# Kernel optimization log

Hardware: AMD Instinct MI355X
Metric: run time of the kernel (lower is better)

Reference implementation:

```python
import jax, jax.numpy as jnp
import numpy as np
import math

JOINT_NAMES = ['pelvis', 'hip_R', 'hip_L', 'knee_R', 'knee_L', 'ankle_R', 'ankle_L', 'trunk', 'shoulder_R', 'shoulder_L', 'elbow_R', 'elbow_L']
KINEMATIC_CHAINS = {'pelvis': ['hip_R', 'hip_L', 'trunk'], 'hip_R': ['pelvis', 'knee_R'], 'hip_L': ['pelvis', 'knee_L'], 'knee_R': ['hip_R', 'ankle_R'], 'knee_L': ['hip_L', 'ankle_L'], 'ankle_R': ['knee_R'], 'ankle_L': ['knee_L'], 'trunk': ['pelvis', 'shoulder_R', 'shoulder_L'], 'shoulder_R': ['trunk', 'elbow_R'], 'shoulder_L': ['trunk', 'elbow_L'], 'elbow_R': ['shoulder_R'], 'elbow_L': ['shoulder_L']}

D_MODEL = 128
N_HEADS = 4
HEAD_DIM = D_MODEL // N_HEADS
B = 16384
N = 12

def build_adjacency_matrix():
    n = len(JOINT_NAMES)
    adj = np.zeros((n, n), dtype=np.float32)
    idx = {name: i for i, name in enumerate(JOINT_NAMES)}
    for joint, neighbors in KINEMATIC_CHAINS.items():
        i = idx[joint]
        for nb in neighbors:
            j = idx[nb]
            adj[i, j] = 1.0
            adj[j, i] = 1.0
    adj = adj + np.eye(n, dtype=np.float32)
    return jnp.asarray(adj)

def setup_inputs() -> dict:
    key = jax.random.key(0)
    ks = jax.random.split(key, 12)
    s = 1.0 / math.sqrt(D_MODEL)  # torch Linear default init scale
    inp = {
        'x': jax.random.normal(ks[0], (B, N, D_MODEL), dtype=jnp.float32),
        'visibility': jax.random.uniform(ks[1], (B, N), dtype=jnp.float32),
        'Wq': jax.random.uniform(ks[2], (D_MODEL, D_MODEL), jnp.float32, -s, s),
        'bq': jax.random.uniform(ks[3], (D_MODEL,), jnp.float32, -s, s),
        'Wk': jax.random.uniform(ks[4], (D_MODEL, D_MODEL), jnp.float32, -s, s),
        'bk': jax.random.uniform(ks[5], (D_MODEL,), jnp.float32, -s, s),
        'Wv': jax.random.uniform(ks[6], (D_MODEL, D_MODEL), jnp.float32, -s, s),
        'bv': jax.random.uniform(ks[7], (D_MODEL,), jnp.float32, -s, s),
        'Wo': jax.random.uniform(ks[8], (D_MODEL, D_MODEL), jnp.float32, -s, s),
        'bo': jax.random.uniform(ks[9], (D_MODEL,), jnp.float32, -s, s),
        'bias_scale': jnp.asarray(1.0, dtype=jnp.float32),
        'adjacency': build_adjacency_matrix(),
    }
    return inp

def reference(x, visibility, Wq, bq, Wk, bk, Wv, bv, Wo, bo, bias_scale, adjacency):
    Bsz, Nj, D = x.shape
    # projections; weights stored as (out,in) like torch Linear -> x @ W.T + b
    def proj(W, b):
        return (jnp.einsum('bnd,ed->bne', x, W) + b).reshape(Bsz, Nj, N_HEADS, HEAD_DIM).transpose(0, 2, 1, 3)
    q = proj(Wq, bq)  # (B, H, N, hd)
    k = proj(Wk, bk)
    v = proj(Wv, bv)
    scores = jnp.einsum('bhnd,bhmd->bhnm', q, k) / math.sqrt(HEAD_DIM)
    scores = scores + adjacency[None, None, :, :] * bias_scale
    # visibility mask: subtract 10 where key joint is not visible
    scores = scores - 10.0 * (1.0 - visibility[:, None, None, :])
    attn = jax.nn.softmax(scores, axis=-1)
    out = jnp.einsum('bhnm,bhmd->bhnd', attn, v)
    out = out.transpose(0, 2, 1, 3).reshape(Bsz, Nj, D)
    out = jnp.einsum('bnd,ed->bne', out, Wo) + bo
    return out
```

## Files before the change

kernel.cpp:

```cpp
#include <hip/hip_runtime.h>


typedef unsigned short u16;
typedef short bf16x8 __attribute__((ext_vector_type(8)));
typedef float f32x4 __attribute__((ext_vector_type(4)));

#define MFMA(a, b, c) __builtin_amdgcn_mfma_f32_16x16x32_bf16((a), (b), (c), 0, 0, 0)

#define BPW   4
#define ROWS  (BPW * 12)
#define XPAD  136

struct SMem {
    u16   xs[ROWS * XPAD];
    u16   qs[ROWS * XPAD];
    u16   ks[ROWS * XPAD];
    u16   vT[BPW * 128 * 32];
    u16   P[4 * 16 * 32];
    float bias_s[16 * 16];
    float vis_s[BPW * 16];
    float bvec[4 * 128];
};

__device__ __forceinline__ u16 f2b(float f) {
    unsigned u = __builtin_bit_cast(unsigned, f);
    return (u16)((u + 0x7fffu + ((u >> 16) & 1u)) >> 16);
}

__device__ __forceinline__ void st4(u16* p, float a, float b, float c, float d) {
    ushort4 v; v.x = f2b(a); v.y = f2b(b); v.z = f2b(c); v.w = f2b(d);
    *(ushort4*)p = v;
}

__global__ void prep_w(const float* __restrict__ Wq, const float* __restrict__ Wk,
                       const float* __restrict__ Wv, const float* __restrict__ Wo,
                       u16* __restrict__ wbf) {
    int i = blockIdx.x * 256 + threadIdx.x;
    wbf[i]         = f2b(Wq[i]);
    wbf[16384 + i] = f2b(Wk[i]);
    wbf[32768 + i] = f2b(Wv[i]);
    wbf[49152 + i] = f2b(Wo[i]);
}

__global__ __launch_bounds__(256, 2) void cja_main(
    const float* __restrict__ x, const float* __restrict__ vis,
    const float* __restrict__ bq, const float* __restrict__ bk,
    const float* __restrict__ bv, const float* __restrict__ bo,
    const float* __restrict__ bias_scale, const float* __restrict__ adj,
    const u16* __restrict__ wbf, float* __restrict__ out)
{
    extern __shared__ char smraw[];
    SMem& sm = *(SMem*)smraw;

    const int tid  = threadIdx.x;
    const int wave = tid >> 6;
    const int lane = tid & 63;
    const int lq   = lane >> 4;
    const int lm   = lane & 15;
    const int b0   = blockIdx.x * BPW;

    for (int i = tid; i < ROWS * 32; i += 256) {
        int row = i >> 5, c4 = (i & 31) << 2;
        float4 v = *(const float4*)(x + ((size_t)(b0 * 12 + row) << 7) + c4);
        st4(sm.xs + row * XPAD + c4, v.x, v.y, v.z, v.w);
    }
    for (int i = tid; i < BPW * 128; i += 256) {
        unsigned* d = (unsigned*)(sm.vT + i * 32 + 12);
        #pragma unroll
        for (int j = 0; j < 10; j++) d[j] = 0u;
    }
    if (tid < 64) {
        unsigned* d = (unsigned*)(sm.P + tid * 32 + 16);
        #pragma unroll
        for (int j = 0; j < 8; j++) d[j] = 0u;
    }
    {
        float scale = bias_scale[0];
        int n = tid >> 4, m = tid & 15;
        float bval = -1e30f;
        if (n < 12 && m < 12) bval = adj[n * 12 + m] * scale;
        sm.bias_s[tid] = bval;
        if (tid < BPW * 16) {
            int bb = tid >> 4, mm = tid & 15;
            sm.vis_s[tid] = (mm < 12) ? vis[(size_t)(b0 + bb) * 12 + mm] : 1.0f;
        }
        if (tid < 128) {
            sm.bvec[tid]       = bq[tid];
            sm.bvec[128 + tid] = bk[tid];
            sm.bvec[256 + tid] = bv[tid];
            sm.bvec[384 + tid] = bo[tid];
        }
    }
    __syncthreads();

    {
        const u16* Wq_b = wbf;
        const u16* Wk_b = wbf + 16384;
        const u16* Wv_b = wbf + 32768;
        f32x4 accq[2][3], acck[2][3], accv[3][2];
        #pragma unroll
        for (int i = 0; i < 2; i++)
            #pragma unroll
            for (int j = 0; j < 3; j++) { accq[i][j] = (f32x4){0,0,0,0}; acck[i][j] = (f32x4){0,0,0,0}; }
        #pragma unroll
        for (int i = 0; i < 3; i++)
            #pragma unroll
            for (int j = 0; j < 2; j++) accv[i][j] = (f32x4){0,0,0,0};

        const int mrow0 = (wave * 2) * 16 + lm;
        const int mrow1 = mrow0 + 16;
        #pragma unroll
        for (int ks = 0; ks < 4; ks++) {
            const int koff = ks * 32 + lq * 8;
            bf16x8 xf[3];
            #pragma unroll
            for (int nt = 0; nt < 3; nt++)
                xf[nt] = *(const bf16x8*)(sm.xs + (nt * 16 + lm) * XPAD + koff);
            bf16x8 wq0 = *(const bf16x8*)(Wq_b + mrow0 * 128 + koff);
            bf16x8 wq1 = *(const bf16x8*)(Wq_b + mrow1 * 128 + koff);
            bf16x8 wk0 = *(const bf16x8*)(Wk_b + mrow0 * 128 + koff);
            bf16x8 wk1 = *(const bf16x8*)(Wk_b + mrow1 * 128 + koff);
            bf16x8 wv0 = *(const bf16x8*)(Wv_b + mrow0 * 128 + koff);
            bf16x8 wv1 = *(const bf16x8*)(Wv_b + mrow1 * 128 + koff);
            #pragma unroll
            for (int nt = 0; nt < 3; nt++) {
                accq[0][nt] = MFMA(wq0, xf[nt], accq[0][nt]);
                accq[1][nt] = MFMA(wq1, xf[nt], accq[1][nt]);
                acck[0][nt] = MFMA(wk0, xf[nt], acck[0][nt]);
                acck[1][nt] = MFMA(wk1, xf[nt], acck[1][nt]);
                accv[nt][0] = MFMA(xf[nt], wv0, accv[nt][0]);
                accv[nt][1] = MFMA(xf[nt], wv1, accv[nt][1]);
            }
        }
        #pragma unroll
        for (int mi = 0; mi < 2; mi++) {
            const int e0 = (wave * 2 + mi) * 16 + lq * 4;
            float bq0 = sm.bvec[e0], bq1 = sm.bvec[e0+1], bq2 = sm.bvec[e0+2], bq3 = sm.bvec[e0+3];
            float bk0 = sm.bvec[128+e0], bk1 = sm.bvec[128+e0+1], bk2 = sm.bvec[128+e0+2], bk3 = sm.bvec[128+e0+3];
            #pragma unroll
            for (int nt = 0; nt < 3; nt++) {
                const int n = nt * 16 + lm;
                st4(sm.qs + n * XPAD + e0, accq[mi][nt][0]+bq0, accq[mi][nt][1]+bq1,
                                           accq[mi][nt][2]+bq2, accq[mi][nt][3]+bq3);
                st4(sm.ks + n * XPAD + e0, acck[mi][nt][0]+bk0, acck[mi][nt][1]+bk1,
                                           acck[mi][nt][2]+bk2, acck[mi][nt][3]+bk3);
            }
        }
        #pragma unroll
        for (int nt2 = 0; nt2 < 2; nt2++) {
            const int e = (wave * 2 + nt2) * 16 + lm;
            const float bvv = sm.bvec[256 + e];
            #pragma unroll
            for (int mt = 0; mt < 3; mt++) {
                #pragma unroll
                for (int r = 0; r < 4; r++) {
                    int n = mt * 16 + lq * 4 + r;
                    int bb = n / 12, j = n - bb * 12;
                    sm.vT[bb * 4096 + e * 32 + j] = f2b(accv[mt][nt2][r] + bvv);
                }
            }
        }
    }
    __syncthreads();

    {
        const int bl = wave;
        const int nql  = (lm < 12) ? lm : 11;
        const int qrow = (bl * 12 + nql) * XPAD;
        const float vism = 10.0f * (1.0f - sm.vis_s[bl * 16 + lm]);
        u16* Pw = sm.P + wave * 512;
        #pragma unroll
        for (int h = 0; h < 4; h++) {
            bf16x8 qa = *(const bf16x8*)(sm.qs + qrow + h * 32 + lq * 8);
            bf16x8 kb = *(const bf16x8*)(sm.ks + qrow + h * 32 + lq * 8);
            f32x4 sc = (f32x4){0,0,0,0};
            sc = MFMA(qa, kb, sc);
            float p[4];
            #pragma unroll
            for (int r = 0; r < 4; r++) {
                const int n = lq * 4 + r;
                float s = sc[r] * 0.17677669529663689f + sm.bias_s[n * 16 + lm] - vism;
                float mx = s;
                mx = fmaxf(mx, __shfl_xor(mx, 1, 16));
                mx = fmaxf(mx, __shfl_xor(mx, 2, 16));
                mx = fmaxf(mx, __shfl_xor(mx, 4, 16));
                mx = fmaxf(mx, __shfl_xor(mx, 8, 16));
                float e = __expf(s - mx);
                float l = e;
                l += __shfl_xor(l, 1, 16);
                l += __shfl_xor(l, 2, 16);
                l += __shfl_xor(l, 4, 16);
                l += __shfl_xor(l, 8, 16);
                p[r] = e / l;
            }
            #pragma unroll
            for (int r = 0; r < 4; r++)
                Pw[(lq * 4 + r) * 32 + lm] = (lm < 12) ? f2b(p[r]) : (u16)0;
            #pragma unroll
            for (int mt = 0; mt < 2; mt++) {
                bf16x8 va = *(const bf16x8*)(sm.vT + bl * 4096 + (h * 32 + mt * 16 + lm) * 32 + lq * 8);
                bf16x8 pb = *(const bf16x8*)(Pw + lm * 32 + lq * 8);
                f32x4 c = (f32x4){0,0,0,0};
                c = MFMA(va, pb, c);
                if (lm < 12) {
                    u16* d = sm.xs + (bl * 12 + lm) * XPAD + h * 32 + mt * 16 + lq * 4;
                    st4(d, c[0], c[1], c[2], c[3]);
                }
            }
        }
    }
    __syncthreads();

    {
        const u16* Wo_b = wbf + 49152;
        f32x4 acc[2][3];
        #pragma unroll
        for (int i = 0; i < 2; i++)
            #pragma unroll
            for (int j = 0; j < 3; j++) acc[i][j] = (f32x4){0,0,0,0};
        const int m0 = (wave * 2) * 16 + lm;
        #pragma unroll
        for (int ks = 0; ks < 4; ks++) {
            const int koff = ks * 32 + lq * 8;
            bf16x8 a0 = *(const bf16x8*)(Wo_b + m0 * 128 + koff);
            bf16x8 a1 = *(const bf16x8*)(Wo_b + (m0 + 16) * 128 + koff);
            #pragma unroll
            for (int nt = 0; nt < 3; nt++) {
                bf16x8 bfr = *(const bf16x8*)(sm.xs + (nt * 16 + lm) * XPAD + koff);
                acc[0][nt] = MFMA(a0, bfr, acc[0][nt]);
                acc[1][nt] = MFMA(a1, bfr, acc[1][nt]);
            }
        }
        #pragma unroll
        for (int mi = 0; mi < 2; mi++) {
            const int e0 = (wave * 2 + mi) * 16 + lq * 4;
            float bo0 = sm.bvec[384+e0], bo1 = sm.bvec[384+e0+1],
                  bo2 = sm.bvec[384+e0+2], bo3 = sm.bvec[384+e0+3];
            #pragma unroll
            for (int nt = 0; nt < 3; nt++) {
                const int n = nt * 16 + lm;
                float4 o;
                o.x = acc[mi][nt][0] + bo0;
                o.y = acc[mi][nt][1] + bo1;
                o.z = acc[mi][nt][2] + bo2;
                o.w = acc[mi][nt][3] + bo3;
                *(float4*)(out + ((size_t)(b0 * 12 + n) << 7) + e0) = o;
            }
        }
    }
}

extern "C" void kernel_launch(void* const* d_in, const int* in_sizes, int n_in,
                              void* d_out, int out_size, void* d_ws, size_t ws_size,
                              hipStream_t stream) {
    const float* x   = (const float*)d_in[0];
    const float* vis = (const float*)d_in[1];
    const float* Wq  = (const float*)d_in[2];
    const float* bq  = (const float*)d_in[3];
    const float* Wk  = (const float*)d_in[4];
    const float* bk  = (const float*)d_in[5];
    const float* Wv  = (const float*)d_in[6];
    const float* bv  = (const float*)d_in[7];
    const float* Wo  = (const float*)d_in[8];
    const float* bo  = (const float*)d_in[9];
    const float* bs  = (const float*)d_in[10];
    const float* adj = (const float*)d_in[11];
    u16* wbf = (u16*)d_ws;

    prep_w<<<64, 256, 0, stream>>>(Wq, Wk, Wv, Wo, wbf);
    cja_main<<<16384 / BPW, 256, sizeof(SMem), stream>>>(
        x, vis, bq, bk, bv, bo, bs, adj, wbf, (float*)d_out);
}
```

Before: 294.5 us.

## Load x directly from global into MFMA fragments and shrink shared memory footprint

Drops the shared-memory staging buffer for x: each wave reads fp32 x straight from global memory and packs it into bf16 fragments for the QKV projection, and the attention output now reuses the qs buffer. The vT and P buffers get smaller padded strides, which cuts LDS size enough for the launch bound to be raised to 3 blocks per CU. Softmax switches to exp2 with log2(e) folded into the scale, bias and visibility terms, skips the max subtraction, and applies the normalising reciprocal after the PV MFMA. The risks are redundant global reads of x across waves and possible overflow, since the softmax no longer subtracts the row max.

```diff
diff --git a/kernel.cpp b/kernel.cpp
--- a/kernel.cpp
+++ b/kernel.cpp
@@ -3,6 +3,7 @@
 
 typedef unsigned short u16;
 typedef short bf16x8 __attribute__((ext_vector_type(8)));
+typedef short bf16x4 __attribute__((ext_vector_type(4)));
 typedef float f32x4 __attribute__((ext_vector_type(4)));
 
 #define MFMA(a, b, c) __builtin_amdgcn_mfma_f32_16x16x32_bf16((a), (b), (c), 0, 0, 0)
@@ -10,16 +11,18 @@
 #define BPW   4
 #define ROWS  (BPW * 12)
 #define XPAD  136
+#define VPAD  20
+#define PPAD  20
 
 struct SMem {
-    u16   xs[ROWS * XPAD];
     u16   qs[ROWS * XPAD];
     u16   ks[ROWS * XPAD];
-    u16   vT[BPW * 128 * 32];
-    u16   P[4 * 16 * 32];
+    u16   vT[BPW * 128 * VPAD];
+    u16   P[4 * 16 * PPAD];
     float bias_s[16 * 16];
     float vis_s[BPW * 16];
     float bvec[4 * 128];
+    float rls[4 * 16];
 };
 
 __device__ __forceinline__ u16 f2b(float f) {
@@ -30,6 +33,15 @@
 __device__ __forceinline__ void st4(u16* p, float a, float b, float c, float d) {
     ushort4 v; v.x = f2b(a); v.y = f2b(b); v.z = f2b(c); v.w = f2b(d);
     *(ushort4*)p = v;
+}
+
+__device__ __forceinline__ bf16x8 pack8(float4 a, float4 b) {
+    bf16x8 r;
+    r[0] = (short)f2b(a.x); r[1] = (short)f2b(a.y);
+    r[2] = (short)f2b(a.z); r[3] = (short)f2b(a.w);
+    r[4] = (short)f2b(b.x); r[5] = (short)f2b(b.y);
+    r[6] = (short)f2b(b.z); r[7] = (short)f2b(b.w);
+    return r;
 }
 
 __global__ void prep_w(const float* __restrict__ Wq, const float* __restrict__ Wk,
@@ -42,7 +54,7 @@
     wbf[49152 + i] = f2b(Wo[i]);
 }
 
-__global__ __launch_bounds__(256, 2) void cja_main(
+__global__ __launch_bounds__(256, 3) void cja_main(
     const float* __restrict__ x, const float* __restrict__ vis,
     const float* __restrict__ bq, const float* __restrict__ bk,
     const float* __restrict__ bv, const float* __restrict__ bo,
@@ -59,30 +71,23 @@
     const int lm   = lane & 15;
     const int b0   = blockIdx.x * BPW;
 
-    for (int i = tid; i < ROWS * 32; i += 256) {
-        int row = i >> 5, c4 = (i & 31) << 2;
-        float4 v = *(const float4*)(x + ((size_t)(b0 * 12 + row) << 7) + c4);
-        st4(sm.xs + row * XPAD + c4, v.x, v.y, v.z, v.w);
-    }
     for (int i = tid; i < BPW * 128; i += 256) {
-        unsigned* d = (unsigned*)(sm.vT + i * 32 + 12);
-        #pragma unroll
-        for (int j = 0; j < 10; j++) d[j] = 0u;
-    }
-    if (tid < 64) {
-        unsigned* d = (unsigned*)(sm.P + tid * 32 + 16);
-        #pragma unroll
-        for (int j = 0; j < 8; j++) d[j] = 0u;
-    }
-    {
-        float scale = bias_scale[0];
+        unsigned* d = (unsigned*)(sm.vT + i * VPAD + 12);
+        d[0] = 0u; d[1] = 0u; d[2] = 0u; d[3] = 0u;
+    }
+    {
+        const float L2E = 1.4426950408889634f;
+        float scale = bias_scale[0] * L2E;
         int n = tid >> 4, m = tid & 15;
-        float bval = -1e30f;
-        if (n < 12 && m < 12) bval = adj[n * 12 + m] * scale;
+        float bval;
+        if (m >= 12)     bval = -1e30f;
+        else if (n < 12) bval = adj[n * 12 + m] * scale;
+        else             bval = 0.0f;
         sm.bias_s[tid] = bval;
         if (tid < BPW * 16) {
             int bb = tid >> 4, mm = tid & 15;
-            sm.vis_s[tid] = (mm < 12) ? vis[(size_t)(b0 + bb) * 12 + mm] : 1.0f;
+            sm.vis_s[tid] = (mm < 12) ? 10.0f * L2E * (1.0f - vis[(size_t)(b0 + bb) * 12 + mm])
+                                      : 0.0f;
         }
         if (tid < 128) {
             sm.bvec[tid]       = bq[tid];
@@ -97,6 +102,7 @@
         const u16* Wq_b = wbf;
         const u16* Wk_b = wbf + 16384;
         const u16* Wv_b = wbf + 32768;
+        const float* xw = x + (size_t)b0 * 1536;
         f32x4 accq[2][3], acck[2][3], accv[3][2];
         #pragma unroll
         for (int i = 0; i < 2; i++)
@@ -107,15 +113,19 @@
             #pragma unroll
             for (int j = 0; j < 2; j++) accv[i][j] = (f32x4){0,0,0,0};
 
-        const int mrow0 = (wave * 2) * 16 + lm;
+        const int mrow0 = wave * 32 + lm;
         const int mrow1 = mrow0 + 16;
         #pragma unroll
-        for (int ks = 0; ks < 4; ks++) {
-            const int koff = ks * 32 + lq * 8;
+        for (int ks2 = 0; ks2 < 4; ks2++) {
+            const int koff = ks2 * 32 + lq * 8;
             bf16x8 xf[3];
             #pragma unroll
-            for (int nt = 0; nt < 3; nt++)
-                xf[nt] = *(const bf16x8*)(sm.xs + (nt * 16 + lm) * XPAD + koff);
+            for (int nt = 0; nt < 3; nt++) {
+                const float* xp = xw + (nt * 16 + lm) * 128 + koff;
+                float4 u0 = *(const float4*)xp;
+                float4 u1 = *(const float4*)(xp + 4);
+                xf[nt] = pack8(u0, u1);
+            }
             bf16x8 wq0 = *(const bf16x8*)(Wq_b + mrow0 * 128 + koff);
             bf16x8 wq1 = *(const bf16x8*)(Wq_b + mrow1 * 128 + koff);
             bf16x8 wk0 = *(const bf16x8*)(Wk_b + mrow0 * 128 + koff);
@@ -156,7 +166,7 @@
                 for (int r = 0; r < 4; r++) {
                     int n = mt * 16 + lq * 4 + r;
                     int bb = n / 12, j = n - bb * 12;
-                    sm.vT[bb * 4096 + e * 32 + j] = f2b(accv[mt][nt2][r] + bvv);
+                    sm.vT[bb * (128 * VPAD) + e * VPAD + j] = f2b(accv[mt][nt2][r] + bvv);
                 }
             }
         }
@@ -164,47 +174,53 @@
     __syncthreads();
 
     {
-        const int bl = wave;
+        const int bl   = wave;
         const int nql  = (lm < 12) ? lm : 11;
-        const int qrow = (bl * 12 + nql) * XPAD;
-        const float vism = 10.0f * (1.0f - sm.vis_s[bl * 16 + lm]);
-        u16* Pw = sm.P + wave * 512;
+        const u16* qrowp = sm.qs + (bl * 12 + nql) * XPAD;
+        const u16* krowp = sm.ks + (bl * 12 + nql) * XPAD;
+        const float vism = sm.vis_s[bl * 16 + lm];
+        float bias_b[4];
+        #pragma unroll
+        for (int r = 0; r < 4; r++) bias_b[r] = sm.bias_s[(lq * 4 + r) * 16 + lm];
+        u16*   Pw  = sm.P + wave * (16 * PPAD);
+        float* rlw = sm.rls + wave * 16;
+        const u16* vTb = sm.vT + bl * (128 * VPAD);
+        const float SC2 = 0.2550348606381560f;
+        const bf16x8 z8 = {0,0,0,0,0,0,0,0};
         #pragma unroll
         for (int h = 0; h < 4; h++) {
-            bf16x8 qa = *(const bf16x8*)(sm.qs + qrow + h * 32 + lq * 8);
-            bf16x8 kb = *(const bf16x8*)(sm.ks + qrow + h * 32 + lq * 8);
-            f32x4 sc = (f32x4){0,0,0,0};
-            sc = MFMA(qa, kb, sc);
-            float p[4];
+            bf16x8 qa = *(const bf16x8*)(qrowp + h * 32 + lq * 8);
+            bf16x8 kb = *(const bf16x8*)(krowp + h * 32 + lq * 8);
+            f32x4 sc = MFMA(qa, kb, ((f32x4){0,0,0,0}));
             #pragma unroll
             for (int r = 0; r < 4; r++) {
-                const int n = lq * 4 + r;
-                float s = sc[r] * 0.17677669529663689f + sm.bias_s[n * 16 + lm] - vism;
-                float mx = s;
-                mx = fmaxf(mx, __shfl_xor(mx, 1, 16));
-                mx = fmaxf(mx, __shfl_xor(mx, 2, 16));
-                mx = fmaxf(mx, __shfl_xor(mx, 4, 16));
-                mx = fmaxf(mx, __shfl_xor(mx, 8, 16));
-                float e = __expf(s - mx);
-                float l = e;
+                float s2 = sc[r] * SC2 + bias_b[r] - vism;
+                float e  = __builtin_amdgcn_exp2f(s2);
+                float l  = e;
                 l += __shfl_xor(l, 1, 16);
                 l += __shfl_xor(l, 2, 16);
                 l += __shfl_xor(l, 4, 16);
                 l += __shfl_xor(l, 8, 16);
-                p[r] = e / l;
-            }
-            #pragma unroll
-            for (int r = 0; r < 4; r++)
-                Pw[(lq * 4 + r) * 32 + lm] = (lm < 12) ? f2b(p[r]) : (u16)0;
+                Pw[(lq * 4 + r) * PPAD + lm] = f2b(e);
+                if (lm == 0) rlw[lq * 4 + r] = __builtin_amdgcn_rcpf(l);
+            }
+            float rln = rlw[lm];
+            bf16x8 pb = z8;
+            if (lq < 2) {
+                const bf16x4* pp = (const bf16x4*)(Pw + lm * PPAD + lq * 8);
+                pb = __builtin_shufflevector(pp[0], pp[1], 0, 1, 2, 3, 4, 5, 6, 7);
+            }
             #pragma unroll
             for (int mt = 0; mt < 2; mt++) {
-                bf16x8 va = *(const bf16x8*)(sm.vT + bl * 4096 + (h * 32 + mt * 16 + lm) * 32 + lq * 8);
-                bf16x8 pb = *(const bf16x8*)(Pw + lm * 32 + lq * 8);
-                f32x4 c = (f32x4){0,0,0,0};
-                c = MFMA(va, pb, c);
+                bf16x8 va = z8;
+                if (lq < 2) {
+                    const bf16x4* vp = (const bf16x4*)(vTb + (h * 32 + mt * 16 + lm) * VPAD + lq * 8);
+                    va = __builtin_shufflevector(vp[0], vp[1], 0, 1, 2, 3, 4, 5, 6, 7);
+                }
+                f32x4 c = MFMA(va, pb, ((f32x4){0,0,0,0}));
                 if (lm < 12) {
-                    u16* d = sm.xs + (bl * 12 + lm) * XPAD + h * 32 + mt * 16 + lq * 4;
-                    st4(d, c[0], c[1], c[2], c[3]);
+                    u16* d = sm.qs + (bl * 12 + lm) * XPAD + h * 32 + mt * 16 + lq * 4;
+                    st4(d, c[0] * rln, c[1] * rln, c[2] * rln, c[3] * rln);
                 }
             }
         }
@@ -218,15 +234,15 @@
         for (int i = 0; i < 2; i++)
             #pragma unroll
             for (int j = 0; j < 3; j++) acc[i][j] = (f32x4){0,0,0,0};
-        const int m0 = (wave * 2) * 16 + lm;
-        #pragma unroll
-        for (int ks = 0; ks < 4; ks++) {
-            const int koff = ks * 32 + lq * 8;
+        const int m0 = wave * 32 + lm;
+        #pragma unroll
+        for (int ks2 = 0; ks2 < 4; ks2++) {
+            const int koff = ks2 * 32 + lq * 8;
             bf16x8 a0 = *(const bf16x8*)(Wo_b + m0 * 128 + koff);
             bf16x8 a1 = *(const bf16x8*)(Wo_b + (m0 + 16) * 128 + koff);
             #pragma unroll
             for (int nt = 0; nt < 3; nt++) {
-                bf16x8 bfr = *(const bf16x8*)(sm.xs + (nt * 16 + lm) * XPAD + koff);
+                bf16x8 bfr = *(const bf16x8*)(sm.qs + (nt * 16 + lm) * XPAD + koff);
                 acc[0][nt] = MFMA(a0, bfr, acc[0][nt]);
                 acc[1][nt] = MFMA(a1, bfr, acc[1][nt]);
             }
```

Measured after the change: 287.2 us. 1.03x faster.
